# Performance work log

Hardware: AMD Instinct MI355X
Metric: run time of the kernel (lower is better)

The kernel has to match this reference:

```python
import jax, jax.numpy as jnp
import numpy as np

B, NX, NH, NY, K = 4096, 512, 512, 256, 8


def setup_inputs() -> dict:
    key = jax.random.key(0)
    k0, k1, k2, k3, k4, k5 = jax.random.split(key, 6)
    s = 1.0 / np.sqrt(NH)  # torch RNNCell init scale
    x = jax.random.normal(k0, (B, NX), jnp.float32)
    h = jax.random.normal(k1, (B, NH), jnp.float32)
    pi = jax.random.uniform(k2, (B, K), jnp.float32)
    pi = pi / pi.sum(axis=1, keepdims=True)  # __init_belief normalizes to sum 1
    W_ih = jax.random.uniform(k3, (K, NH, NX), jnp.float32, minval=-s, maxval=s)
    W_hh = jax.random.uniform(k4, (K, NH, NH), jnp.float32, minval=-s, maxval=s)
    W_out = jax.random.uniform(k5, (NY, NH), jnp.float32, minval=-s, maxval=s)
    return {"x": x, "h": h, "pi": pi, "W_ih": W_ih, "W_hh": W_hh, "W_out": W_out}


def reference(x, h, pi, W_ih, W_hh, W_out):
    # Per-state RNN cells (bias=False): h_k[:, :, k] = tanh(x @ W_ih[k].T + h @ W_hh[k].T)
    h_k = jnp.tanh(
        jnp.einsum('bx,knx->bnk', x, W_ih)
        + jnp.einsum('bh,knh->bnk', h, W_hh)
    )  # (B, NH, K)
    # out_k = out_layer applied per state: (B, NY, K)
    out_k = jnp.einsum('bnk,yn->byk', h_k, W_out)
    # belief-weighted soft combination of hidden states: states[b] = h_k[b] @ pi[b]
    h_mix = jnp.einsum('bnk,bk->bn', h_k, pi)  # (B, NH)
    out = h_mix @ W_out.T  # (B, NY)
    return (out, h_mix, out_k, h_k)
```

## Files before the change

### kernel.cpp

```cpp
#include <hip/hip_runtime.h>
#include <hip/hip_bf16.h>
#include <stdint.h>

typedef unsigned short u16;
typedef __attribute__((ext_vector_type(8))) short short8;
typedef __attribute__((ext_vector_type(4))) float f32x4;

#define BATCH 4096
#define OFF_OUT  0
#define OFF_HMIX (BATCH * 256)
#define OFF_OK   (OFF_HMIX + BATCH * 512)
#define OFF_HK   (OFF_OK + BATCH * 256 * 8)

#define WS_XB   0
#define WS_HB   (2097152)
#define WS_WIH  (4194304)
#define WS_WHH  (6291456)
#define WS_WOUT (8388608)
#define WS_T    (8519680)
#define WS_OB   (25296896)

__device__ __forceinline__ float b2f(u16 v) {
  union { uint32_t u; float f; } c; c.u = ((uint32_t)v) << 16; return c.f;
}
__device__ __forceinline__ u16 f2b(float f) {
  union { float f; uint32_t u; } c; c.f = f;
  uint32_t u = c.u;
  return (u16)((u + 0x7fffu + ((u >> 16) & 1u)) >> 16);
}

__device__ __forceinline__ void gload16(const u16* g, u16* l) {
  __builtin_amdgcn_global_load_lds(
      (const __attribute__((address_space(1))) void*)g,
      (__attribute__((address_space(3))) void*)l, 16, 0, 0);
}

__global__ __launch_bounds__(256) void k0_cvt(
    const float* __restrict__ x, const float* __restrict__ h,
    const float* __restrict__ Wih, const float* __restrict__ Whh,
    const float* __restrict__ Wout, u16* __restrict__ ws) {
  const int i = blockIdx.x * 256 + threadIdx.x;
  const float* src; int j; size_t dst;
  if      (i <  524288) { src = x;    j = i;           dst = WS_XB;   }
  else if (i < 1048576) { src = h;    j = i -  524288; dst = WS_HB;   }
  else if (i < 1572864) { src = Wih;  j = i - 1048576; dst = WS_WIH;  }
  else if (i < 2097152) { src = Whh;  j = i - 1572864; dst = WS_WHH;  }
  else                  { src = Wout; j = i - 2097152; dst = WS_WOUT; }
  const float4 v = ((const float4*)src)[j];
  ushort4 o;
  o.x = f2b(v.x); o.y = f2b(v.y); o.z = f2b(v.z); o.w = f2b(v.w);
  ((ushort4*)(ws + dst))[j] = o;
}

__global__ __launch_bounds__(512, 2) void k1_gemm_tanh(
    const u16* __restrict__ xb, const u16* __restrict__ hb,
    const u16* __restrict__ Wih, const u16* __restrict__ Whh,
    u16* __restrict__ Tb) {
  __shared__ u16 S[65536];
  const int tid  = threadIdx.x;
  const int lane = tid & 63;
  const int w    = tid >> 6;
  const int wm   = w >> 2;
  const int wn   = w & 3;
  const int quad = lane >> 4, rl = lane & 15, l7 = lane & 7;
  const int sr   = tid >> 3;
  const int sc   = ((tid & 7) ^ (sr & 7)) * 8;

  const int wg  = blockIdx.x;
  const int lin = ((wg & 7) << 5) | (wg >> 3);
  const int bx  = lin & 15;
  const int by  = lin >> 4;
  const int row0 = bx * 256;
  const int col0 = by * 256;
  const int kk   = col0 >> 9;
  const int nh0  = col0 & 511;

  const u16* const As2[2] = { xb, hb };
  const u16* const Bs2[2] = { Wih + (size_t)kk * 262144, Whh + (size_t)kk * 262144 };

  auto stage = [&](int tile, int region) {
    if (tile >= 16) return;
    const int g    = tile >> 3;
    const int ko   = (tile & 7) * 64;
    const int isB  = region >> 1;
    const int half = region & 1;
    const u16* src = isB ? Bs2[g] : As2[g];
    const int r0   = (isB ? nh0 : row0) + half * 128;
    u16* dst = S + (tile & 1) * 32768 + isB * 16384 + half * 8192;
    const u16* s0 = src + (size_t)(r0 + sr) * 512 + ko + sc;
    gload16(s0,            dst + tid * 8);
    gload16(s0 + 64 * 512, dst + 4096 + tid * 8);
  };

  auto ldA = [&](int buf, int mi, int ks) -> short8 {
    return *(const short8*)&S[buf * 32768 +
                              (wm * 128 + mi * 16 + rl) * 64 +
                              ((ks * 4 + quad) ^ l7) * 8];
  };
  auto ldB = [&](int buf, int j, int ks) -> short8 {
    return *(const short8*)&S[buf * 32768 + 16384 +
                              (wn * 64 + j * 16 + rl) * 64 +
                              ((ks * 4 + quad) ^ l7) * 8];
  };

  f32x4 acc[8][4] = {};
  short8 af[4][2], bf[4][2];

  stage(0, 0); stage(0, 1); stage(0, 2); stage(0, 3); stage(1, 0);
  asm volatile("s_waitcnt vmcnt(2)" ::: "memory");
  __builtin_amdgcn_s_barrier();

#pragma unroll 1
  for (int t = 0; t < 16; ++t) {
    const int buf = t & 1;

#pragma unroll
    for (int m = 0; m < 4; ++m) { af[m][0] = ldA(buf, m, 0); af[m][1] = ldA(buf, m, 1); }
#pragma unroll
    for (int j = 0; j < 2; ++j) { bf[j][0] = ldB(buf, j, 0); bf[j][1] = ldB(buf, j, 1); }
    stage(t + 1, 1);
    __builtin_amdgcn_s_barrier();
    asm volatile("s_waitcnt lgkmcnt(0)" ::: "memory");
    __builtin_amdgcn_s_setprio(1);
#pragma unroll
    for (int m = 0; m < 4; ++m)
#pragma unroll
      for (int n = 0; n < 2; ++n)
#pragma unroll
        for (int ks = 0; ks < 2; ++ks)
          acc[m][n] = __builtin_amdgcn_mfma_f32_16x16x32_bf16(af[m][ks], bf[n][ks], acc[m][n], 0, 0, 0);
    __builtin_amdgcn_s_setprio(0);
    __builtin_amdgcn_s_barrier();

#pragma unroll
    for (int j = 2; j < 4; ++j) { bf[j][0] = ldB(buf, j, 0); bf[j][1] = ldB(buf, j, 1); }
    stage(t + 1, 2);
    __builtin_amdgcn_s_barrier();
    asm volatile("s_waitcnt lgkmcnt(0)" ::: "memory");
    __builtin_amdgcn_s_setprio(1);
#pragma unroll
    for (int m = 0; m < 4; ++m)
#pragma unroll
      for (int n = 2; n < 4; ++n)
#pragma unroll
        for (int ks = 0; ks < 2; ++ks)
          acc[m][n] = __builtin_amdgcn_mfma_f32_16x16x32_bf16(af[m][ks], bf[n][ks], acc[m][n], 0, 0, 0);
    __builtin_amdgcn_s_setprio(0);
    __builtin_amdgcn_s_barrier();

#pragma unroll
    for (int m = 0; m < 4; ++m) { af[m][0] = ldA(buf, 4 + m, 0); af[m][1] = ldA(buf, 4 + m, 1); }
    stage(t + 1, 3);
    __builtin_amdgcn_s_barrier();
    asm volatile("s_waitcnt lgkmcnt(0)" ::: "memory");
    __builtin_amdgcn_s_setprio(1);
#pragma unroll
    for (int m = 0; m < 4; ++m)
#pragma unroll
      for (int n = 2; n < 4; ++n)
#pragma unroll
        for (int ks = 0; ks < 2; ++ks)
          acc[4 + m][n] = __builtin_amdgcn_mfma_f32_16x16x32_bf16(af[m][ks], bf[n][ks], acc[4 + m][n], 0, 0, 0);
    __builtin_amdgcn_s_setprio(0);
    __builtin_amdgcn_s_barrier();

    stage(t + 2, 0);
    __builtin_amdgcn_s_barrier();
    __builtin_amdgcn_s_setprio(1);
#pragma unroll
    for (int m = 0; m < 4; ++m)
#pragma unroll
      for (int n = 0; n < 2; ++n)
#pragma unroll
        for (int ks = 0; ks < 2; ++ks)
          acc[4 + m][n] = __builtin_amdgcn_mfma_f32_16x16x32_bf16(af[m][ks], bf[n][ks], acc[4 + m][n], 0, 0, 0);
    __builtin_amdgcn_s_setprio(0);
    if (t < 14) asm volatile("s_waitcnt vmcnt(2)" ::: "memory");
    else        asm volatile("s_waitcnt vmcnt(0)" ::: "memory");
    __builtin_amdgcn_s_barrier();
  }

#pragma unroll 1
  for (int hp = 0; hp < 2; ++hp) {
    if (wm == hp) {
#pragma unroll
      for (int m = 0; m < 8; ++m)
#pragma unroll
        for (int n = 0; n < 4; ++n)
#pragma unroll
          for (int r = 0; r < 4; ++r) {
            const int lr = m * 16 + quad * 4 + r;
            const float v = acc[m][n][r];
            const float e = __expf(2.0f * v);
            S[lr * 264 + wn * 64 + n * 16 + rl] = f2b(1.0f - 2.0f / (e + 1.0f));
          }
    }
    asm volatile("s_waitcnt lgkmcnt(0)" ::: "memory");
    __builtin_amdgcn_s_barrier();
#pragma unroll
    for (int p = 0; p < 8; ++p) {
      const int idx = p * 512 + tid;
      const int c = idx & 31, rr = idx >> 5;
      *(short8*)&Tb[(size_t)(row0 + hp * 128 + rr) * 4096 + col0 + c * 8] =
          *(const short8*)&S[rr * 264 + c * 8];
    }
    __builtin_amdgcn_s_barrier();
  }
}

__global__ __launch_bounds__(256) void k2_gemm_out(
    const u16* __restrict__ Tb, const u16* __restrict__ Wout,
    u16* __restrict__ Ob) {
  __shared__ u16 S[128 * 136];
  u16* As = S;
  u16* Bs = S + 128 * 64;
  const int tid  = threadIdx.x;
  const int lane = tid & 63;
  const int w    = tid >> 6;
  const int wm   = w >> 1, wn = w & 1;
  const int row0 = blockIdx.x * 128;
  const int y0   = blockIdx.y * 128;
  const int kk   = blockIdx.z;
  const int sr   = tid >> 3;
  const int sc   = ((tid & 7) ^ ((tid >> 3) & 7)) * 8;
  const int ldsw = (w * 8) * 64;

  f32x4 acc[4][4] = {};

  for (int kt = 0; kt < 8; ++kt) {
    const int kb = kt * 64;
#pragma unroll
    for (int ro = 0; ro < 4; ++ro) {
      gload16(Tb + (size_t)(row0 + ro * 32 + sr) * 4096 + kk * 512 + kb + sc,
              &As[ro * 32 * 64 + ldsw]);
      gload16(Wout + (size_t)(y0 + ro * 32 + sr) * 512 + kb + sc,
              &Bs[ro * 32 * 64 + ldsw]);
    }
    __syncthreads();
    const int l7 = lane & 7, quad = lane >> 4, rl = lane & 15;
#pragma unroll
    for (int ks = 0; ks < 2; ++ks) {
      short8 af[4], bf[4];
      const int cs = ((ks * 4 + quad) ^ l7) * 8;
#pragma unroll
      for (int i = 0; i < 4; ++i)
        af[i] = *(const short8*)&As[(wm * 64 + i * 16 + rl) * 64 + cs];
#pragma unroll
      for (int j = 0; j < 4; ++j)
        bf[j] = *(const short8*)&Bs[(wn * 64 + j * 16 + rl) * 64 + cs];
#pragma unroll
      for (int i = 0; i < 4; ++i)
#pragma unroll
        for (int j = 0; j < 4; ++j)
          acc[i][j] = __builtin_amdgcn_mfma_f32_16x16x32_bf16(af[i], bf[j], acc[i][j], 0, 0, 0);
    }
    __syncthreads();
  }

  const int quad = lane >> 4, cl = lane & 15;
#pragma unroll
  for (int i = 0; i < 4; ++i)
#pragma unroll
    for (int j = 0; j < 4; ++j)
#pragma unroll
      for (int r = 0; r < 4; ++r) {
        const int row = wm * 64 + i * 16 + quad * 4 + r;
        const int col = wn * 64 + j * 16 + cl;
        S[row * 136 + col] = f2b(acc[i][j][r]);
      }
  __syncthreads();
#pragma unroll
  for (int it = 0; it < 8; ++it) {
    const int idx = it * 256 + tid;
    const int c = idx & 15;
    const int r = idx >> 4;
    *(short8*)&Ob[(size_t)(row0 + r) * 2048 + kk * 256 + y0 + c * 8] =
        *(const short8*)&S[r * 136 + c * 8];
  }
}

__global__ __launch_bounds__(512) void k3_epi(const float* __restrict__ pi,
                                              const u16* __restrict__ Tb,
                                              const u16* __restrict__ Ob,
                                              float* __restrict__ dout) {
  const int b   = blockIdx.x;
  const int tid = threadIdx.x;

  float pif[8];
#pragma unroll
  for (int k = 0; k < 8; ++k) pif[k] = pi[b * 8 + k];

  float tv[8]; float hm = 0.0f;
#pragma unroll
  for (int k = 0; k < 8; ++k) {
    const float v = b2f(Tb[(size_t)b * 4096 + k * 512 + tid]);
    tv[k] = v; hm += pif[k] * v;
  }
  float4* tw = (float4*)&dout[OFF_HK + (size_t)b * 4096 + tid * 8];
  tw[0] = make_float4(tv[0], tv[1], tv[2], tv[3]);
  tw[1] = make_float4(tv[4], tv[5], tv[6], tv[7]);
  dout[OFF_HMIX + (size_t)b * 512 + tid] = hm;

  if (tid < 256) {
    float ov[8]; float om = 0.0f;
#pragma unroll
    for (int k = 0; k < 8; ++k) {
      const float v = b2f(Ob[(size_t)b * 2048 + k * 256 + tid]);
      ov[k] = v; om += pif[k] * v;
    }
    float4* ow = (float4*)&dout[OFF_OK + (size_t)b * 2048 + tid * 8];
    ow[0] = make_float4(ov[0], ov[1], ov[2], ov[3]);
    ow[1] = make_float4(ov[4], ov[5], ov[6], ov[7]);
    dout[OFF_OUT + (size_t)b * 256 + tid] = om;
  }
}

extern "C" void kernel_launch(void* const* d_in, const int* in_sizes, int n_in,
                              void* d_out, int out_size, void* d_ws, size_t ws_size,
                              hipStream_t stream) {
  const float* x    = (const float*)d_in[0];
  const float* h    = (const float*)d_in[1];
  const float* pi   = (const float*)d_in[2];
  const float* Wih  = (const float*)d_in[3];
  const float* Whh  = (const float*)d_in[4];
  const float* Wout = (const float*)d_in[5];
  float* out = (float*)d_out;
  u16* ws  = (u16*)d_ws;

  k0_cvt<<<dim3(8320), 256, 0, stream>>>(x, h, Wih, Whh, Wout, ws);
  k1_gemm_tanh<<<dim3(256), 512, 0, stream>>>(
      ws + WS_XB, ws + WS_HB, ws + WS_WIH, ws + WS_WHH, ws + WS_T);
  k2_gemm_out<<<dim3(32, 2, 8), 256, 0, stream>>>(ws + WS_T, ws + WS_WOUT, ws + WS_OB);
  k3_epi<<<dim3(BATCH), 512, 0, stream>>>(pi, ws + WS_T, ws + WS_OB, out);
}
```

Measured before the change: 215.4 us.

## Fuse per-state output GEMM into tanh GEMM kernel with full-NH tiles

Retiles the first GEMM so each workgroup owns 128 batch rows and all 512 hidden units of one state, which lets the tanh output stay in LDS. The second GEMM (h_k times W_out) then runs in the same kernel, reading A from LDS and W_out straight from global memory, so the separate k2 launch and its re-read of the tanh tensor are gone. The A tile is single-buffered while the B tiles stay double-buffered, and the priority hints are removed. In exchange, the fused workgroups use more LDS, each one performs a serial second GEMM whose W_out loads come from global without staging, and tiles are smaller in the batch dimension.

```diff
diff --git a/kernel.cpp b/kernel.cpp
--- a/kernel.cpp
+++ b/kernel.cpp
@@ -52,11 +52,12 @@
   ((ushort4*)(ws + dst))[j] = o;
 }
 
-__global__ __launch_bounds__(512, 2) void k1_gemm_tanh(
+__global__ __launch_bounds__(512, 2) void k1_fused(
     const u16* __restrict__ xb, const u16* __restrict__ hb,
     const u16* __restrict__ Wih, const u16* __restrict__ Whh,
-    u16* __restrict__ Tb) {
-  __shared__ u16 S[65536];
+    const u16* __restrict__ Wout, u16* __restrict__ Tb,
+    u16* __restrict__ Ob) {
+  __shared__ u16 S[73728];
   const int tid  = threadIdx.x;
   const int lane = tid & 63;
   const int w    = tid >> 6;
@@ -66,216 +67,181 @@
   const int sr   = tid >> 3;
   const int sc   = ((tid & 7) ^ (sr & 7)) * 8;
 
-  const int wg  = blockIdx.x;
-  const int lin = ((wg & 7) << 5) | (wg >> 3);
-  const int bx  = lin & 15;
-  const int by  = lin >> 4;
-  const int row0 = bx * 256;
-  const int col0 = by * 256;
-  const int kk   = col0 >> 9;
-  const int nh0  = col0 & 511;
+  const int wg   = blockIdx.x;
+  const int kk   = wg & 7;
+  const int bx   = wg >> 3;
+  const int row0 = bx * 128;
 
   const u16* const As2[2] = { xb, hb };
   const u16* const Bs2[2] = { Wih + (size_t)kk * 262144, Whh + (size_t)kk * 262144 };
 
-  auto stage = [&](int tile, int region) {
+  auto stageB = [&](int tile, int r) {
     if (tile >= 16) return;
-    const int g    = tile >> 3;
-    const int ko   = (tile & 7) * 64;
-    const int isB  = region >> 1;
-    const int half = region & 1;
-    const u16* src = isB ? Bs2[g] : As2[g];
-    const int r0   = (isB ? nh0 : row0) + half * 128;
-    u16* dst = S + (tile & 1) * 32768 + isB * 16384 + half * 8192;
-    const u16* s0 = src + (size_t)(r0 + sr) * 512 + ko + sc;
-    gload16(s0,            dst + tid * 8);
-    gload16(s0 + 64 * 512, dst + 4096 + tid * 8);
+    const int g = tile >> 3, ko = (tile & 7) * 64;
+    gload16(Bs2[g] + (size_t)(r * 64 + sr) * 512 + ko + sc,
+            S + 8192 + (tile & 1) * 32768 + r * 4096 + tid * 8);
   };
-
-  auto ldA = [&](int buf, int mi, int ks) -> short8 {
-    return *(const short8*)&S[buf * 32768 +
-                              (wm * 128 + mi * 16 + rl) * 64 +
+  auto stageA = [&](int tile, int r) {
+    if (tile >= 16) return;
+    const int g = tile >> 3, ko = (tile & 7) * 64;
+    gload16(As2[g] + (size_t)(row0 + r * 64 + sr) * 512 + ko + sc,
+            S + r * 4096 + tid * 8);
+  };
+  auto ldA = [&](int mi, int ks) -> short8 {
+    return *(const short8*)&S[(wm * 64 + mi * 16 + rl) * 64 +
                               ((ks * 4 + quad) ^ l7) * 8];
   };
-  auto ldB = [&](int buf, int j, int ks) -> short8 {
-    return *(const short8*)&S[buf * 32768 + 16384 +
-                              (wn * 64 + j * 16 + rl) * 64 +
+  auto ldB = [&](int buf, int nj, int ks) -> short8 {
+    return *(const short8*)&S[8192 + buf * 32768 +
+                              (wn * 128 + nj * 16 + rl) * 64 +
                               ((ks * 4 + quad) ^ l7) * 8];
   };
 
-  f32x4 acc[8][4] = {};
-  short8 af[4][2], bf[4][2];
-
-  stage(0, 0); stage(0, 1); stage(0, 2); stage(0, 3); stage(1, 0);
-  asm volatile("s_waitcnt vmcnt(2)" ::: "memory");
+  f32x4 acc[4][8] = {};
+
+  stageA(0, 0); stageA(0, 1);
+#pragma unroll
+  for (int r = 0; r < 8; ++r) stageB(0, r);
+  asm volatile("s_waitcnt vmcnt(0)" ::: "memory");
   __builtin_amdgcn_s_barrier();
 
 #pragma unroll 1
   for (int t = 0; t < 16; ++t) {
     const int buf = t & 1;
-
-#pragma unroll
-    for (int m = 0; m < 4; ++m) { af[m][0] = ldA(buf, m, 0); af[m][1] = ldA(buf, m, 1); }
+    short8 al[4][2], bf[2][2];
+
+#pragma unroll
+    for (int m = 0; m < 4; ++m) { al[m][0] = ldA(m, 0); al[m][1] = ldA(m, 1); }
 #pragma unroll
     for (int j = 0; j < 2; ++j) { bf[j][0] = ldB(buf, j, 0); bf[j][1] = ldB(buf, j, 1); }
-    stage(t + 1, 1);
+    stageB(t + 1, 0); stageB(t + 1, 1);
     __builtin_amdgcn_s_barrier();
     asm volatile("s_waitcnt lgkmcnt(0)" ::: "memory");
-    __builtin_amdgcn_s_setprio(1);
 #pragma unroll
     for (int m = 0; m < 4; ++m)
 #pragma unroll
       for (int n = 0; n < 2; ++n)
 #pragma unroll
         for (int ks = 0; ks < 2; ++ks)
-          acc[m][n] = __builtin_amdgcn_mfma_f32_16x16x32_bf16(af[m][ks], bf[n][ks], acc[m][n], 0, 0, 0);
-    __builtin_amdgcn_s_setprio(0);
-    __builtin_amdgcn_s_barrier();
-
-#pragma unroll
-    for (int j = 2; j < 4; ++j) { bf[j][0] = ldB(buf, j, 0); bf[j][1] = ldB(buf, j, 1); }
-    stage(t + 1, 2);
+          acc[m][n] = __builtin_amdgcn_mfma_f32_16x16x32_bf16(al[m][ks], bf[n][ks], acc[m][n], 0, 0, 0);
+    __builtin_amdgcn_s_barrier();
+
+#pragma unroll
+    for (int j = 0; j < 2; ++j) { bf[j][0] = ldB(buf, 2 + j, 0); bf[j][1] = ldB(buf, 2 + j, 1); }
+    stageA(t + 1, 0); stageA(t + 1, 1);
+    stageB(t + 1, 2); stageB(t + 1, 3);
     __builtin_amdgcn_s_barrier();
     asm volatile("s_waitcnt lgkmcnt(0)" ::: "memory");
-    __builtin_amdgcn_s_setprio(1);
 #pragma unroll
     for (int m = 0; m < 4; ++m)
 #pragma unroll
-      for (int n = 2; n < 4; ++n)
-#pragma unroll
-        for (int ks = 0; ks < 2; ++ks)
-          acc[m][n] = __builtin_amdgcn_mfma_f32_16x16x32_bf16(af[m][ks], bf[n][ks], acc[m][n], 0, 0, 0);
-    __builtin_amdgcn_s_setprio(0);
-    __builtin_amdgcn_s_barrier();
-
-#pragma unroll
-    for (int m = 0; m < 4; ++m) { af[m][0] = ldA(buf, 4 + m, 0); af[m][1] = ldA(buf, 4 + m, 1); }
-    stage(t + 1, 3);
+      for (int n = 0; n < 2; ++n)
+#pragma unroll
+        for (int ks = 0; ks < 2; ++ks)
+          acc[m][2 + n] = __builtin_amdgcn_mfma_f32_16x16x32_bf16(al[m][ks], bf[n][ks], acc[m][2 + n], 0, 0, 0);
+    if (t < 15) asm volatile("s_waitcnt vmcnt(6)" ::: "memory");
+    else        asm volatile("s_waitcnt vmcnt(0)" ::: "memory");
+    __builtin_amdgcn_s_barrier();
+
+#pragma unroll
+    for (int j = 0; j < 2; ++j) { bf[j][0] = ldB(buf, 4 + j, 0); bf[j][1] = ldB(buf, 4 + j, 1); }
+    stageB(t + 1, 4); stageB(t + 1, 5);
     __builtin_amdgcn_s_barrier();
     asm volatile("s_waitcnt lgkmcnt(0)" ::: "memory");
-    __builtin_amdgcn_s_setprio(1);
 #pragma unroll
     for (int m = 0; m < 4; ++m)
 #pragma unroll
-      for (int n = 2; n < 4; ++n)
-#pragma unroll
-        for (int ks = 0; ks < 2; ++ks)
-          acc[4 + m][n] = __builtin_amdgcn_mfma_f32_16x16x32_bf16(af[m][ks], bf[n][ks], acc[4 + m][n], 0, 0, 0);
-    __builtin_amdgcn_s_setprio(0);
-    __builtin_amdgcn_s_barrier();
-
-    stage(t + 2, 0);
-    __builtin_amdgcn_s_barrier();
-    __builtin_amdgcn_s_setprio(1);
+      for (int n = 0; n < 2; ++n)
+#pragma unroll
+        for (int ks = 0; ks < 2; ++ks)
+          acc[m][4 + n] = __builtin_amdgcn_mfma_f32_16x16x32_bf16(al[m][ks], bf[n][ks], acc[m][4 + n], 0, 0, 0);
+    __builtin_amdgcn_s_barrier();
+
+#pragma unroll
+    for (int j = 0; j < 2; ++j) { bf[j][0] = ldB(buf, 6 + j, 0); bf[j][1] = ldB(buf, 6 + j, 1); }
+    stageB(t + 1, 6); stageB(t + 1, 7);
+    __builtin_amdgcn_s_barrier();
+    asm volatile("s_waitcnt lgkmcnt(0)" ::: "memory");
 #pragma unroll
     for (int m = 0; m < 4; ++m)
 #pragma unroll
       for (int n = 0; n < 2; ++n)
 #pragma unroll
         for (int ks = 0; ks < 2; ++ks)
-          acc[4 + m][n] = __builtin_amdgcn_mfma_f32_16x16x32_bf16(af[m][ks], bf[n][ks], acc[4 + m][n], 0, 0, 0);
-    __builtin_amdgcn_s_setprio(0);
-    if (t < 14) asm volatile("s_waitcnt vmcnt(2)" ::: "memory");
+          acc[m][6 + n] = __builtin_amdgcn_mfma_f32_16x16x32_bf16(al[m][ks], bf[n][ks], acc[m][6 + n], 0, 0, 0);
+    if (t < 15) asm volatile("s_waitcnt vmcnt(4)" ::: "memory");
     else        asm volatile("s_waitcnt vmcnt(0)" ::: "memory");
     __builtin_amdgcn_s_barrier();
   }
 
-#pragma unroll 1
-  for (int hp = 0; hp < 2; ++hp) {
-    if (wm == hp) {
-#pragma unroll
-      for (int m = 0; m < 8; ++m)
-#pragma unroll
-        for (int n = 0; n < 4; ++n)
-#pragma unroll
-          for (int r = 0; r < 4; ++r) {
-            const int lr = m * 16 + quad * 4 + r;
-            const float v = acc[m][n][r];
-            const float e = __expf(2.0f * v);
-            S[lr * 264 + wn * 64 + n * 16 + rl] = f2b(1.0f - 2.0f / (e + 1.0f));
-          }
-    }
-    asm volatile("s_waitcnt lgkmcnt(0)" ::: "memory");
-    __builtin_amdgcn_s_barrier();
-#pragma unroll
-    for (int p = 0; p < 8; ++p) {
-      const int idx = p * 512 + tid;
-      const int c = idx & 31, rr = idx >> 5;
-      *(short8*)&Tb[(size_t)(row0 + hp * 128 + rr) * 4096 + col0 + c * 8] =
-          *(const short8*)&S[rr * 264 + c * 8];
-    }
-    __builtin_amdgcn_s_barrier();
-  }
-}
-
-__global__ __launch_bounds__(256) void k2_gemm_out(
-    const u16* __restrict__ Tb, const u16* __restrict__ Wout,
-    u16* __restrict__ Ob) {
-  __shared__ u16 S[128 * 136];
-  u16* As = S;
-  u16* Bs = S + 128 * 64;
-  const int tid  = threadIdx.x;
-  const int lane = tid & 63;
-  const int w    = tid >> 6;
-  const int wm   = w >> 1, wn = w & 1;
-  const int row0 = blockIdx.x * 128;
-  const int y0   = blockIdx.y * 128;
-  const int kk   = blockIdx.z;
-  const int sr   = tid >> 3;
-  const int sc   = ((tid & 7) ^ ((tid >> 3) & 7)) * 8;
-  const int ldsw = (w * 8) * 64;
-
-  f32x4 acc[4][4] = {};
-
-  for (int kt = 0; kt < 8; ++kt) {
-    const int kb = kt * 64;
-#pragma unroll
-    for (int ro = 0; ro < 4; ++ro) {
-      gload16(Tb + (size_t)(row0 + ro * 32 + sr) * 4096 + kk * 512 + kb + sc,
-              &As[ro * 32 * 64 + ldsw]);
-      gload16(Wout + (size_t)(y0 + ro * 32 + sr) * 512 + kb + sc,
-              &Bs[ro * 32 * 64 + ldsw]);
-    }
-    __syncthreads();
-    const int l7 = lane & 7, quad = lane >> 4, rl = lane & 15;
-#pragma unroll
-    for (int ks = 0; ks < 2; ++ks) {
-      short8 af[4], bf[4];
-      const int cs = ((ks * 4 + quad) ^ l7) * 8;
-#pragma unroll
-      for (int i = 0; i < 4; ++i)
-        af[i] = *(const short8*)&As[(wm * 64 + i * 16 + rl) * 64 + cs];
-#pragma unroll
-      for (int j = 0; j < 4; ++j)
-        bf[j] = *(const short8*)&Bs[(wn * 64 + j * 16 + rl) * 64 + cs];
-#pragma unroll
-      for (int i = 0; i < 4; ++i)
-#pragma unroll
-        for (int j = 0; j < 4; ++j)
-          acc[i][j] = __builtin_amdgcn_mfma_f32_16x16x32_bf16(af[i], bf[j], acc[i][j], 0, 0, 0);
-    }
-    __syncthreads();
-  }
-
-  const int quad = lane >> 4, cl = lane & 15;
-#pragma unroll
-  for (int i = 0; i < 4; ++i)
-#pragma unroll
-    for (int j = 0; j < 4; ++j)
+#pragma unroll
+  for (int mi = 0; mi < 4; ++mi)
+#pragma unroll
+    for (int nj = 0; nj < 8; ++nj)
 #pragma unroll
       for (int r = 0; r < 4; ++r) {
-        const int row = wm * 64 + i * 16 + quad * 4 + r;
-        const int col = wn * 64 + j * 16 + cl;
-        S[row * 136 + col] = f2b(acc[i][j][r]);
+        const int row = wm * 64 + mi * 16 + quad * 4 + r;
+        const int col = wn * 128 + nj * 16 + rl;
+        const float v = acc[mi][nj][r];
+        const float e = __expf(2.0f * v);
+        S[row * 520 + col] = f2b(1.0f - 2.0f / (e + 1.0f));
       }
-  __syncthreads();
-#pragma unroll
-  for (int it = 0; it < 8; ++it) {
-    const int idx = it * 256 + tid;
-    const int c = idx & 15;
-    const int r = idx >> 4;
-    *(short8*)&Ob[(size_t)(row0 + r) * 2048 + kk * 256 + y0 + c * 8] =
-        *(const short8*)&S[r * 136 + c * 8];
+  asm volatile("s_waitcnt lgkmcnt(0)" ::: "memory");
+  __builtin_amdgcn_s_barrier();
+
+#pragma unroll
+  for (int p = 0; p < 16; ++p) {
+    const int idx = p * 512 + tid;
+    const int c = idx & 63, rr = idx >> 6;
+    *(short8*)&Tb[(size_t)(row0 + rr) * 4096 + kk * 512 + c * 8] =
+        *(const short8*)&S[rr * 520 + c * 8];
+  }
+
+  f32x4 acc2[4][4] = {};
+#pragma unroll 2
+  for (int c2 = 0; c2 < 8; ++c2) {
+    short8 b2[4][2], a2[4][2];
+#pragma unroll
+    for (int nj = 0; nj < 4; ++nj)
+#pragma unroll
+      for (int ks = 0; ks < 2; ++ks)
+        b2[nj][ks] = *(const short8*)&Wout[(size_t)(wn * 64 + nj * 16 + rl) * 512 +
+                                           c2 * 64 + ks * 32 + quad * 8];
+#pragma unroll
+    for (int mi = 0; mi < 4; ++mi)
+#pragma unroll
+      for (int ks = 0; ks < 2; ++ks)
+        a2[mi][ks] = *(const short8*)&S[(wm * 64 + mi * 16 + rl) * 520 +
+                                        c2 * 64 + ks * 32 + quad * 8];
+#pragma unroll
+    for (int mi = 0; mi < 4; ++mi)
+#pragma unroll
+      for (int nj = 0; nj < 4; ++nj)
+#pragma unroll
+        for (int ks = 0; ks < 2; ++ks)
+          acc2[mi][nj] = __builtin_amdgcn_mfma_f32_16x16x32_bf16(a2[mi][ks], b2[nj][ks], acc2[mi][nj], 0, 0, 0);
+  }
+  asm volatile("s_waitcnt lgkmcnt(0)" ::: "memory");
+  __builtin_amdgcn_s_barrier();
+
+#pragma unroll
+  for (int mi = 0; mi < 4; ++mi)
+#pragma unroll
+    for (int nj = 0; nj < 4; ++nj)
+#pragma unroll
+      for (int r = 0; r < 4; ++r) {
+        const int row = wm * 64 + mi * 16 + quad * 4 + r;
+        const int col = wn * 64 + nj * 16 + rl;
+        S[row * 264 + col] = f2b(acc2[mi][nj][r]);
+      }
+  asm volatile("s_waitcnt lgkmcnt(0)" ::: "memory");
+  __builtin_amdgcn_s_barrier();
+#pragma unroll
+  for (int p = 0; p < 8; ++p) {
+    const int idx = p * 512 + tid;
+    const int c = idx & 31, rr = idx >> 5;
+    *(short8*)&Ob[(size_t)(row0 + rr) * 2048 + kk * 256 + c * 8] =
+        *(const short8*)&S[rr * 264 + c * 8];
   }
 }
 
@@ -328,8 +294,8 @@
   u16* ws  = (u16*)d_ws;
 
   k0_cvt<<<dim3(8320), 256, 0, stream>>>(x, h, Wih, Whh, Wout, ws);
-  k1_gemm_tanh<<<dim3(256), 512, 0, stream>>>(
-      ws + WS_XB, ws + WS_HB, ws + WS_WIH, ws + WS_WHH, ws + WS_T);
-  k2_gemm_out<<<dim3(32, 2, 8), 256, 0, stream>>>(ws + WS_T, ws + WS_WOUT, ws + WS_OB);
+  k1_fused<<<dim3(256), 512, 0, stream>>>(
+      ws + WS_XB, ws + WS_HB, ws + WS_WIH, ws + WS_WHH, ws + WS_WOUT,
+      ws + WS_T, ws + WS_OB);
   k3_epi<<<dim3(BATCH), 512, 0, stream>>>(pi, ws + WS_T, ws + WS_OB, out);
 }
```

New measurement: 214.5 us. Within noise of the previous version (-0.4%).
